# Kernel tuning notes

Hardware: AMD Instinct MI355X
Metric: run time of the kernel (lower is better)

Reference implementation:

```python
import jax, jax.numpy as jnp
import numpy as np

N_NODES = 100000
N_EDGES = 1600000
IN_FEATS = 64
H_FEATS = 64
NUM_CLASSES = 32


def _cgnn(h, e, src, dst, W, b, n_nodes):
    # message: m = h[src] * e  (e is [E,1], broadcasts over feature dim)
    m = h[src] * e  # [E, F]
    # segment mean over destination nodes (DGL fn.mean -> 0 for isolated nodes)
    s = jax.ops.segment_sum(m, dst, num_segments=n_nodes)  # [N, F]
    deg = jax.ops.segment_sum(jnp.ones((m.shape[0],), m.dtype), dst,
                              num_segments=n_nodes)  # [N]
    h_N = s / jnp.maximum(deg, 1.0)[:, None]
    h_total = jnp.concatenate([h, h_N], axis=1)  # [N, 2F]
    return h_total @ W + b


def setup_inputs() -> dict:
    key = jax.random.key(0)
    k = jax.random.split(key, 8)
    in_feat = jax.random.normal(k[0], (N_NODES, IN_FEATS), dtype=jnp.float32)
    edge_feat = jax.random.uniform(k[1], (N_EDGES, 1), dtype=jnp.float32)
    src = jax.random.randint(k[2], (N_EDGES,), 0, N_NODES)
    dst = jax.random.randint(k[3], (N_EDGES,), 0, N_NODES)
    # Linear(2*in_feats, h_feats) and Linear(2*h_feats, num_classes)
    s1 = 1.0 / np.sqrt(2 * IN_FEATS)
    s2 = 1.0 / np.sqrt(2 * H_FEATS)
    W1 = jax.random.uniform(k[4], (2 * IN_FEATS, H_FEATS), jnp.float32, -s1, s1)
    b1 = jax.random.uniform(k[5], (H_FEATS,), jnp.float32, -s1, s1)
    W2 = jax.random.uniform(k[6], (2 * H_FEATS, NUM_CLASSES), jnp.float32, -s2, s2)
    b2 = jax.random.uniform(k[7], (NUM_CLASSES,), jnp.float32, -s2, s2)
    return {"in_feat": in_feat, "edge_feat": edge_feat, "src": src,
            "dst": dst, "W1": W1, "b1": b1, "W2": W2, "b2": b2}


def reference(in_feat, edge_feat, src, dst, W1, b1, W2, b2):
    h = _cgnn(in_feat, edge_feat, src, dst, W1, b1, N_NODES)
    h = jax.nn.relu(h)
    h = _cgnn(h, edge_feat, src, dst, W2, b2, N_NODES)
    return h
```

## Files before the change

### kernel.cpp

```cpp
#include <hip/hip_runtime.h>
#include <hip/hip_bf16.h>


#define F 64
#define EPT 8
#define TPB 1024
#define EPB (EPT * TPB)
#define SBSHIFT 8
#define SBSZ 256
#define NSBMAX 512
#define PADSB 4864

__device__ __forceinline__ unsigned bf16_rne(float f)
{
    unsigned u = __float_as_uint(f);
    return (u + 0x7FFFu + ((u >> 16) & 1u)) >> 16;
}

__global__ __launch_bounds__(256) void cvt_init_kernel(
    const float* __restrict__ x, unsigned short* __restrict__ y, int n8,
    int* __restrict__ bcursor, int nsb)
{
    const int i = blockIdx.x * 256 + threadIdx.x;
    if (i < nsb) bcursor[i] = i * PADSB;
    if (i >= n8) return;
    const float4 a = ((const float4*)x)[2 * i];
    const float4 b = ((const float4*)x)[2 * i + 1];
    uint4 o;
    o.x = bf16_rne(a.x) | (bf16_rne(a.y) << 16);
    o.y = bf16_rne(a.z) | (bf16_rne(a.w) << 16);
    o.z = bf16_rne(b.x) | (bf16_rne(b.y) << 16);
    o.w = bf16_rne(b.z) | (bf16_rne(b.w) << 16);
    ((uint4*)y)[i] = o;
}

__global__ __launch_bounds__(TPB) void multisplit_kernel(
    const int* __restrict__ src, const int* __restrict__ dst,
    const float* __restrict__ ef, int* __restrict__ bcursor,
    int2* __restrict__ brec, int n_edges, int nsb)
{
    __shared__ int lcnt[NSBMAX];
    __shared__ int lbase[NSBMAX];
    const int tid = threadIdx.x;
    for (int i = tid; i < nsb; i += TPB) lcnt[i] = 0;
    __syncthreads();

    const int e0 = blockIdx.x * EPB + tid;
    int d[EPT], rk[EPT];
#pragma unroll
    for (int k = 0; k < EPT; ++k) {
        const int e = e0 + k * TPB;
        const int dd = (e < n_edges) ? dst[e] : -1;
        d[k]  = dd;
        rk[k] = (dd >= 0) ? atomicAdd(&lcnt[dd >> SBSHIFT], 1) : 0;
    }
    __syncthreads();
    for (int i = tid; i < nsb; i += TPB) {
        const int c = lcnt[i];
        lbase[i] = c ? atomicAdd(&bcursor[i], c) : 0;
    }
    __syncthreads();
#pragma unroll
    for (int k = 0; k < EPT; ++k) {
        const int e = e0 + k * TPB;
        if (e < n_edges) {
            const int dd  = d[k];
            const int bkt = dd >> SBSHIFT;
            const int pos = lbase[bkt] + rk[k];
            if (pos < (bkt + 1) * PADSB)
                brec[pos] = make_int2(((dd & (SBSZ - 1)) << 17) | src[e],
                                      __float_as_int(ef[e]));
        }
    }
}

__global__ __launch_bounds__(512) void bucket_sort_kernel(
    int2* __restrict__ brec, const int* __restrict__ bcursor,
    int* __restrict__ off2, int* __restrict__ end2,
    float* __restrict__ invdeg, int n_nodes)
{
    __shared__ int2 stage[PADSB];
    __shared__ int  lcnt[SBSZ];
    __shared__ int  lcur[SBSZ];
    __shared__ int  wsum[4];

    const int b   = blockIdx.x;
    const int tid = threadIdx.x;
    const int w0  = b * PADSB;
    int cnt = bcursor[b] - w0;
    if (cnt > PADSB) cnt = PADSB;

    if (tid < SBSZ) lcnt[tid] = 0;
    __syncthreads();

    for (int i = tid; i < cnt; i += 512) {
        const int2 r = brec[w0 + i];
        stage[i] = r;
        atomicAdd(&lcnt[r.x >> 17], 1);
    }
    __syncthreads();

    int v = 0, c = 0;
    if (tid < SBSZ) {
        c = lcnt[tid];
        v = c;
        for (int d = 1; d < 64; d <<= 1) {
            int t = __shfl_up(v, d, 64);
            if ((tid & 63) >= d) v += t;
        }
        if ((tid & 63) == 63) wsum[tid >> 6] = v;
    }
    __syncthreads();
    if (tid == 0) {
        int a = 0;
#pragma unroll
        for (int i = 0; i < 4; ++i) { int t = wsum[i]; wsum[i] = a; a += t; }
    }
    __syncthreads();
    if (tid < SBSZ) {
        const int excl = wsum[tid >> 6] + (v - c);
        lcur[tid] = excl;
        const int node = (b << SBSHIFT) + tid;
        if (node < n_nodes) {
            off2[node]   = w0 + excl;
            end2[node]   = w0 + excl + c;
            invdeg[node] = 1.0f / fmaxf((float)c, 1.0f);
        }
    }
    __syncthreads();

    for (int i = tid; i < cnt; i += 512) {
        const int2 r   = stage[i];
        const int  pos = atomicAdd(&lcur[r.x >> 17], 1);
        brec[w0 + pos] = make_int2((r.x & 0x1FFFF) << 6, r.y);
    }
}

__global__ __launch_bounds__(256) void agg_h_kernel(
    const unsigned short* __restrict__ hb, const int2* __restrict__ rec,
    const int* __restrict__ off, const int* __restrict__ end,
    const float* __restrict__ invdeg, unsigned short* __restrict__ sb,
    int n_nodes)
{
    const int wid  = (blockIdx.x * 256 + threadIdx.x) >> 6;
    const int lane = threadIdx.x & 63;
    const int n    = lane >> 5;
    const int r    = lane & 31;
    const int g    = r >> 3;
    const int q    = r & 7;

    const int  node   = wid * 2 + n;
    const bool active = node < n_nodes;
    const int  e0 = active ? off[node] : 0;
    const int  e1 = active ? end[node] : 0;

    const char* __restrict__ hq = (const char*)hb + q * 16;

    float4 aA0 = make_float4(0.f, 0.f, 0.f, 0.f);
    float4 aA1 = make_float4(0.f, 0.f, 0.f, 0.f);
    float4 aB0 = make_float4(0.f, 0.f, 0.f, 0.f);
    float4 aB1 = make_float4(0.f, 0.f, 0.f, 0.f);

    for (int base = e0; base < e1; base += 8) {
        const int  eA = base + g;
        const int  eB = base + 4 + g;
        const bool vA = eA < e1;
        const bool vB = eB < e1;
        const int2 rA = rec[vA ? eA : e0];
        const int2 rB = rec[vB ? eB : e0];
        const float evA = vA ? __int_as_float(rA.y) : 0.f;
        const float evB = vB ? __int_as_float(rB.y) : 0.f;
        const uint4 xA = *(const uint4*)(hq + ((size_t)(unsigned)rA.x << 1));
        const uint4 xB = *(const uint4*)(hq + ((size_t)(unsigned)rB.x << 1));

#define ACC8(xa, ev, lo, hi)                                         \
        lo.x = fmaf(__uint_as_float(xa.x << 16),         ev, lo.x);  \
        lo.y = fmaf(__uint_as_float(xa.x & 0xFFFF0000u), ev, lo.y);  \
        lo.z = fmaf(__uint_as_float(xa.y << 16),         ev, lo.z);  \
        lo.w = fmaf(__uint_as_float(xa.y & 0xFFFF0000u), ev, lo.w);  \
        hi.x = fmaf(__uint_as_float(xa.z << 16),         ev, hi.x);  \
        hi.y = fmaf(__uint_as_float(xa.z & 0xFFFF0000u), ev, hi.y);  \
        hi.z = fmaf(__uint_as_float(xa.w << 16),         ev, hi.z);  \
        hi.w = fmaf(__uint_as_float(xa.w & 0xFFFF0000u), ev, hi.w);

        ACC8(xA, evA, aA0, aA1)
        ACC8(xB, evB, aB0, aB1)
    }

    float4 a0 = make_float4(aA0.x + aB0.x, aA0.y + aB0.y,
                            aA0.z + aB0.z, aA0.w + aB0.w);
    float4 a1 = make_float4(aA1.x + aB1.x, aA1.y + aB1.y,
                            aA1.z + aB1.z, aA1.w + aB1.w);

#pragma unroll
    for (int m = 8; m <= 16; m <<= 1) {
        a0.x += __shfl_xor(a0.x, m); a0.y += __shfl_xor(a0.y, m);
        a0.z += __shfl_xor(a0.z, m); a0.w += __shfl_xor(a0.w, m);
        a1.x += __shfl_xor(a1.x, m); a1.y += __shfl_xor(a1.y, m);
        a1.z += __shfl_xor(a1.z, m); a1.w += __shfl_xor(a1.w, m);
    }

    if (g == 0 && active) {
        const float id = invdeg[node];
        uint4 o;
        o.x = bf16_rne(a0.x * id) | (bf16_rne(a0.y * id) << 16);
        o.y = bf16_rne(a0.z * id) | (bf16_rne(a0.w * id) << 16);
        o.z = bf16_rne(a1.x * id) | (bf16_rne(a1.y * id) << 16);
        o.w = bf16_rne(a1.z * id) | (bf16_rne(a1.w * id) << 16);
        *(uint4*)(sb + (size_t)node * F + q * 8) = o;
    }
}

__global__ __launch_bounds__(256) void agg_y_kernel(
    const unsigned short* __restrict__ yb, const int2* __restrict__ rec,
    const int* __restrict__ off, const int* __restrict__ end,
    const float* __restrict__ invdeg, unsigned short* __restrict__ s2b,
    int n_nodes)
{
    const int wid  = (blockIdx.x * 256 + threadIdx.x) >> 6;
    const int lane = threadIdx.x & 63;
    const int n    = lane >> 4;
    const int r    = lane & 15;
    const int g    = r >> 2;
    const int q    = r & 3;

    const int  node   = wid * 4 + n;
    const bool active = node < n_nodes;
    const int  e0 = active ? off[node] : 0;
    const int  e1 = active ? end[node] : 0;

    const char* __restrict__ hq = (const char*)yb + q * 16;

    float4 aA0 = make_float4(0.f, 0.f, 0.f, 0.f);
    float4 aA1 = make_float4(0.f, 0.f, 0.f, 0.f);
    float4 aB0 = make_float4(0.f, 0.f, 0.f, 0.f);
    float4 aB1 = make_float4(0.f, 0.f, 0.f, 0.f);

    for (int base = e0; base < e1; base += 8) {
        const int  eA = base + g;
        const int  eB = base + 4 + g;
        const bool vA = eA < e1;
        const bool vB = eB < e1;
        const int2 rA = rec[vA ? eA : e0];
        const int2 rB = rec[vB ? eB : e0];
        const float evA = vA ? __int_as_float(rA.y) : 0.f;
        const float evB = vB ? __int_as_float(rB.y) : 0.f;
        const uint4 xA = *(const uint4*)(hq + (size_t)(unsigned)rA.x);
        const uint4 xB = *(const uint4*)(hq + (size_t)(unsigned)rB.x);

        ACC8(xA, evA, aA0, aA1)
        ACC8(xB, evB, aB0, aB1)
    }

    float4 a0 = make_float4(aA0.x + aB0.x, aA0.y + aB0.y,
                            aA0.z + aB0.z, aA0.w + aB0.w);
    float4 a1 = make_float4(aA1.x + aB1.x, aA1.y + aB1.y,
                            aA1.z + aB1.z, aA1.w + aB1.w);

#pragma unroll
    for (int m = 4; m <= 8; m <<= 1) {
        a0.x += __shfl_xor(a0.x, m); a0.y += __shfl_xor(a0.y, m);
        a0.z += __shfl_xor(a0.z, m); a0.w += __shfl_xor(a0.w, m);
        a1.x += __shfl_xor(a1.x, m); a1.y += __shfl_xor(a1.y, m);
        a1.z += __shfl_xor(a1.z, m); a1.w += __shfl_xor(a1.w, m);
    }
#undef ACC8

    if (g == 0 && active) {
        const float id = invdeg[node];
        uint4 o;
        o.x = bf16_rne(a0.x * id) | (bf16_rne(a0.y * id) << 16);
        o.y = bf16_rne(a0.z * id) | (bf16_rne(a0.w * id) << 16);
        o.z = bf16_rne(a1.x * id) | (bf16_rne(a1.y * id) << 16);
        o.w = bf16_rne(a1.z * id) | (bf16_rne(a1.w * id) << 16);
        *(uint4*)(s2b + (size_t)node * 32 + q * 8) = o;
    }
}

template <int OUT, bool RELU, bool OUT_BF16>
__global__ __launch_bounds__(256) void linear_lds_kernel(
    const unsigned short* __restrict__ hin_b,
    const unsigned short* __restrict__ sb,
    const float* __restrict__ W, const float* __restrict__ b,
    float* __restrict__ out, unsigned short* __restrict__ hb_out, int n_nodes)
{
    constexpr int JT  = OUT / 4;
    constexpr int STR = 132;
    __shared__ float xin[64 * STR];

    const int tid   = threadIdx.x;
    const int node0 = blockIdx.x * 64;

#define STAGE_BF16(srcp, base_off, width)                                 \
    for (int i = tid; i < 64 * ((width) / 8); i += 256) {                 \
        const int ln = i / ((width) / 8), c8 = i % ((width) / 8);         \
        const int node = node0 + ln;                                      \
        uint4 v = make_uint4(0u, 0u, 0u, 0u);                             \
        if (node < n_nodes)                                               \
            v = *(const uint4*)&srcp[(size_t)node * (width) + c8 * 8];    \
        float4 lo = make_float4(__uint_as_float(v.x << 16),               \
                                __uint_as_float(v.x & 0xFFFF0000u),       \
                                __uint_as_float(v.y << 16),               \
                                __uint_as_float(v.y & 0xFFFF0000u));      \
        float4 hi = make_float4(__uint_as_float(v.z << 16),               \
                                __uint_as_float(v.z & 0xFFFF0000u),       \
                                __uint_as_float(v.w << 16),               \
                                __uint_as_float(v.w & 0xFFFF0000u));      \
        *(float4*)&xin[ln * STR + (base_off) + c8 * 8]     = lo;          \
        *(float4*)&xin[ln * STR + (base_off) + c8 * 8 + 4] = hi;          \
    }

    STAGE_BF16(hin_b, 0, 64)
    STAGE_BF16(sb,    F, 64)
    __syncthreads();

    const int lane = tid & 63;
    const int j0   = __builtin_amdgcn_readfirstlane((tid >> 6) * JT);

    float acc[JT];
#pragma unroll
    for (int j = 0; j < JT; ++j) acc[j] = b[j0 + j];

    const float* __restrict__ xrow = &xin[lane * STR];
#pragma unroll 2
    for (int k4 = 0; k4 < 32; ++k4) {
        const float4 xv = *(const float4*)&xrow[k4 * 4];
#pragma unroll
        for (int kk = 0; kk < 4; ++kk) {
            const int   k  = k4 * 4 + kk;
            const float xk = ((const float*)&xv)[kk];
#pragma unroll
            for (int j = 0; j < JT; ++j)
                acc[j] = fmaf(xk, W[k * OUT + j0 + j], acc[j]);
        }
    }

    const int node = node0 + lane;
    if (node < n_nodes) {
#pragma unroll
        for (int j = 0; j < JT; ++j) {
            float v = acc[j];
            if (RELU) v = fmaxf(v, 0.f);
            acc[j] = v;
        }
        if constexpr (OUT_BF16) {
            unsigned* __restrict__ hw =
                (unsigned*)(hb_out + (size_t)node * OUT + j0);
#pragma unroll
            for (int j = 0; j < JT; j += 2)
                hw[j >> 1] = bf16_rne(acc[j]) | (bf16_rne(acc[j + 1]) << 16);
        } else {
#pragma unroll
            for (int j = 0; j < JT; ++j)
                out[(size_t)node * OUT + j0 + j] = acc[j];
        }
    }
}

__global__ __launch_bounds__(256) void y2gemm_kernel(
    const unsigned short* __restrict__ hin_b, const float* __restrict__ Wb,
    unsigned short* __restrict__ yb2, int n_nodes)
{
    constexpr int STR = 68;
    __shared__ float xin[64 * STR];
    const int tid   = threadIdx.x;
    const int node0 = blockIdx.x * 64;

    STAGE_BF16(hin_b, 0, 64)
    __syncthreads();

    const int lane = tid & 63;
    const int j0   = __builtin_amdgcn_readfirstlane((tid >> 6) * 8);

    float acc[8];
#pragma unroll
    for (int j = 0; j < 8; ++j) acc[j] = 0.f;

    const float* __restrict__ xrow = &xin[lane * STR];
#pragma unroll 2
    for (int k4 = 0; k4 < 16; ++k4) {
        const float4 xv = *(const float4*)&xrow[k4 * 4];
#pragma unroll
        for (int kk = 0; kk < 4; ++kk) {
            const int   k  = k4 * 4 + kk;
            const float xk = ((const float*)&xv)[kk];
#pragma unroll
            for (int j = 0; j < 8; ++j)
                acc[j] = fmaf(xk, Wb[k * 32 + j0 + j], acc[j]);
        }
    }

    const int node = node0 + lane;
    if (node < n_nodes) {
        unsigned* __restrict__ hw = (unsigned*)(yb2 + (size_t)node * 32 + j0);
#pragma unroll
        for (int j = 0; j < 8; j += 2)
            hw[j >> 1] = bf16_rne(acc[j]) | (bf16_rne(acc[j + 1]) << 16);
    }
}

__global__ __launch_bounds__(256) void lin2h_kernel(
    const unsigned short* __restrict__ hin_b,
    const unsigned short* __restrict__ s2b,
    const float* __restrict__ Wt, const float* __restrict__ b,
    float* __restrict__ out, int n_nodes)
{
    constexpr int STR = 100;
    __shared__ float xin[64 * STR];
    const int tid   = threadIdx.x;
    const int node0 = blockIdx.x * 64;

    STAGE_BF16(hin_b, 0,  64)
    STAGE_BF16(s2b,   64, 32)
#undef STAGE_BF16
    __syncthreads();

    const int lane = tid & 63;
    const int j0   = __builtin_amdgcn_readfirstlane((tid >> 6) * 8);

    float acc[8];
#pragma unroll
    for (int j = 0; j < 8; ++j) acc[j] = b[j0 + j];

    const float* __restrict__ xrow = &xin[lane * STR];
#pragma unroll 2
    for (int k4 = 0; k4 < 16; ++k4) {
        const float4 xv = *(const float4*)&xrow[k4 * 4];
#pragma unroll
        for (int kk = 0; kk < 4; ++kk) {
            const int   k  = k4 * 4 + kk;
            const float xk = ((const float*)&xv)[kk];
#pragma unroll
            for (int j = 0; j < 8; ++j)
                acc[j] = fmaf(xk, Wt[k * 32 + j0 + j], acc[j]);
        }
    }

    const int node = node0 + lane;
    if (node < n_nodes) {
#pragma unroll
        for (int j = 0; j < 8; ++j)
            out[(size_t)node * 32 + j0 + j] = acc[j] + xrow[64 + j0 + j];
    }
}

extern "C" void kernel_launch(void* const* d_in, const int* in_sizes, int n_in,
                              void* d_out, int out_size, void* d_ws, size_t ws_size,
                              hipStream_t stream)
{
    const float* in_feat   = (const float*)d_in[0];
    const float* edge_feat = (const float*)d_in[1];
    const int*   src       = (const int*)d_in[2];
    const int*   dst       = (const int*)d_in[3];
    const float* W1        = (const float*)d_in[4];
    const float* b1        = (const float*)d_in[5];
    const float* W2        = (const float*)d_in[6];
    const float* b2        = (const float*)d_in[7];
    float*       out       = (float*)d_out;

    const int n_nodes = in_sizes[0] / F;
    const int n_edges = in_sizes[2];
    const int nsb     = (n_nodes + SBSZ - 1) >> SBSHIFT;

    const int S = 100352;
    int*   wsi     = (int*)d_ws;
    int*   bcursor = wsi;
    int*   off2    = wsi + 1024;
    int*   end2    = wsi + 1024 + S;
    float* invdeg  = (float*)(wsi + 1024 + 2 * S);
    int2*  brec    = (int2*)(wsi + 1024 + 3 * S);
    unsigned short* sb  = (unsigned short*)(brec + (size_t)nsb * PADSB);
    unsigned short* hb0 = sb  + (size_t)n_nodes * F;
    unsigned short* hb1 = hb0 + (size_t)n_nodes * F;
    unsigned short* yb2 = hb1 + (size_t)n_nodes * F;
    unsigned short* s2b = yb2 + (size_t)n_nodes * 32;

    const int n8     = (n_nodes * F) >> 3;
    const int cgrid  = (n8 + 255) / 256;
    const int egrid  = (n_edges + EPB - 1) / EPB;
    const int agrid1 = (n_nodes + 7) / 8;
    const int agrid2 = (n_nodes + 15) / 16;
    const int lgrid  = (n_nodes + 63) / 64;

    cvt_init_kernel<<<cgrid, 256, 0, stream>>>(in_feat, hb0, n8, bcursor, nsb);
    multisplit_kernel<<<egrid, TPB, 0, stream>>>(src, dst, edge_feat,
                                                 bcursor, brec, n_edges, nsb);
    bucket_sort_kernel<<<nsb, 512, 0, stream>>>(brec, bcursor, off2, end2,
                                                invdeg, n_nodes);

    agg_h_kernel<<<agrid1, 256, 0, stream>>>(hb0, brec, off2, end2, invdeg,
                                             sb, n_nodes);
    linear_lds_kernel<64, true, true><<<lgrid, 256, 0, stream>>>(
        hb0, sb, W1, b1, nullptr, hb1, n_nodes);

    y2gemm_kernel<<<lgrid, 256, 0, stream>>>(hb1, W2 + 64 * 32, yb2, n_nodes);
    agg_y_kernel<<<agrid2, 256, 0, stream>>>(yb2, brec, off2, end2, invdeg,
                                             s2b, n_nodes);
    lin2h_kernel<<<lgrid, 256, 0, stream>>>(hb1, s2b, W2, b2, out, n_nodes);
}
```

Measured before the change: 153.1 us.

## Pack edge records into 32-bit words and fuse layer-1 linear with y2 GEMM

Edge records are compressed from int2 (8 bytes) to a single 32-bit word holding a 17-bit source index and a 15-bit bf16 edge weight with the sign bit dropped. This halves record traffic in both aggregation passes. The layer-1 linear+ReLU kernel now also computes the h1·W2b projection from LDS, which removes a separate kernel launch and a re-read of hb1. The cost is extra rounding of edge weights to bf16 and a reliance on edge weights being non-negative and node indices fitting in 17 bits.

```diff
diff --git a/kernel.cpp b/kernel.cpp
--- a/kernel.cpp
+++ b/kernel.cpp
@@ -15,6 +15,11 @@
 {
     unsigned u = __float_as_uint(f);
     return (u + 0x7FFFu + ((u >> 16) & 1u)) >> 16;
+}
+
+__device__ __forceinline__ float rec_ef(unsigned rec)
+{
+    return __uint_as_float((rec & 0xFFFE0000u) >> 1);
 }
 
 __global__ __launch_bounds__(256) void cvt_init_kernel(
@@ -75,9 +80,9 @@
 }
 
 __global__ __launch_bounds__(512) void bucket_sort_kernel(
-    int2* __restrict__ brec, const int* __restrict__ bcursor,
-    int* __restrict__ off2, int* __restrict__ end2,
-    float* __restrict__ invdeg, int n_nodes)
+    const int2* __restrict__ brec, const int* __restrict__ bcursor,
+    unsigned* __restrict__ rec2, int* __restrict__ off2,
+    int* __restrict__ end2, float* __restrict__ invdeg, int n_nodes)
 {
     __shared__ int2 stage[PADSB];
     __shared__ int  lcnt[SBSZ];
@@ -132,12 +137,13 @@
     for (int i = tid; i < cnt; i += 512) {
         const int2 r   = stage[i];
         const int  pos = atomicAdd(&lcur[r.x >> 17], 1);
-        brec[w0 + pos] = make_int2((r.x & 0x1FFFF) << 6, r.y);
+        const unsigned ef15 = bf16_rne(__int_as_float(r.y)) & 0x7FFFu;
+        rec2[w0 + pos] = (ef15 << 17) | (unsigned)(r.x & 0x1FFFF);
     }
 }
 
 __global__ __launch_bounds__(256) void agg_h_kernel(
-    const unsigned short* __restrict__ hb, const int2* __restrict__ rec,
+    const unsigned short* __restrict__ hb, const unsigned* __restrict__ rec,
     const int* __restrict__ off, const int* __restrict__ end,
     const float* __restrict__ invdeg, unsigned short* __restrict__ sb,
     int n_nodes)
@@ -166,12 +172,12 @@
         const int  eB = base + 4 + g;
         const bool vA = eA < e1;
         const bool vB = eB < e1;
-        const int2 rA = rec[vA ? eA : e0];
-        const int2 rB = rec[vB ? eB : e0];
-        const float evA = vA ? __int_as_float(rA.y) : 0.f;
-        const float evB = vB ? __int_as_float(rB.y) : 0.f;
-        const uint4 xA = *(const uint4*)(hq + ((size_t)(unsigned)rA.x << 1));
-        const uint4 xB = *(const uint4*)(hq + ((size_t)(unsigned)rB.x << 1));
+        const unsigned rA = rec[vA ? eA : e0];
+        const unsigned rB = rec[vB ? eB : e0];
+        const float evA = vA ? rec_ef(rA) : 0.f;
+        const float evB = vB ? rec_ef(rB) : 0.f;
+        const uint4 xA = *(const uint4*)(hq + ((size_t)(rA & 0x1FFFFu) << 7));
+        const uint4 xB = *(const uint4*)(hq + ((size_t)(rB & 0x1FFFFu) << 7));
 
 #define ACC8(xa, ev, lo, hi)                                         \
         lo.x = fmaf(__uint_as_float(xa.x << 16),         ev, lo.x);  \
@@ -212,7 +218,7 @@
 }
 
 __global__ __launch_bounds__(256) void agg_y_kernel(
-    const unsigned short* __restrict__ yb, const int2* __restrict__ rec,
+    const unsigned short* __restrict__ yb, const unsigned* __restrict__ rec,
     const int* __restrict__ off, const int* __restrict__ end,
     const float* __restrict__ invdeg, unsigned short* __restrict__ s2b,
     int n_nodes)
@@ -241,16 +247,17 @@
         const int  eB = base + 4 + g;
         const bool vA = eA < e1;
         const bool vB = eB < e1;
-        const int2 rA = rec[vA ? eA : e0];
-        const int2 rB = rec[vB ? eB : e0];
-        const float evA = vA ? __int_as_float(rA.y) : 0.f;
-        const float evB = vB ? __int_as_float(rB.y) : 0.f;
-        const uint4 xA = *(const uint4*)(hq + (size_t)(unsigned)rA.x);
-        const uint4 xB = *(const uint4*)(hq + (size_t)(unsigned)rB.x);
+        const unsigned rA = rec[vA ? eA : e0];
+        const unsigned rB = rec[vB ? eB : e0];
+        const float evA = vA ? rec_ef(rA) : 0.f;
+        const float evB = vB ? rec_ef(rB) : 0.f;
+        const uint4 xA = *(const uint4*)(hq + ((size_t)(rA & 0x1FFFFu) << 6));
+        const uint4 xB = *(const uint4*)(hq + ((size_t)(rB & 0x1FFFFu) << 6));
 
         ACC8(xA, evA, aA0, aA1)
         ACC8(xB, evB, aB0, aB1)
     }
+#undef ACC8
 
     float4 a0 = make_float4(aA0.x + aB0.x, aA0.y + aB0.y,
                             aA0.z + aB0.z, aA0.w + aB0.w);
@@ -264,7 +271,6 @@
         a1.x += __shfl_xor(a1.x, m); a1.y += __shfl_xor(a1.y, m);
         a1.z += __shfl_xor(a1.z, m); a1.w += __shfl_xor(a1.w, m);
     }
-#undef ACC8
 
     if (g == 0 && active) {
         const float id = invdeg[node];
@@ -277,49 +283,56 @@
     }
 }
 
-template <int OUT, bool RELU, bool OUT_BF16>
-__global__ __launch_bounds__(256) void linear_lds_kernel(
-    const unsigned short* __restrict__ hin_b,
+template <int WIDTH>
+__device__ __forceinline__ void stage_rows_bf16(
+    const unsigned short* __restrict__ srcp, float* __restrict__ xin,
+    int node0, int n_nodes, int tid, int stride, int base_off)
+{
+    constexpr int C8 = WIDTH / 8;
+    for (int i = tid; i < 64 * C8; i += 256) {
+        const int ln = i / C8, c8 = i % C8;
+        const int node = node0 + ln;
+        uint4 v = make_uint4(0u, 0u, 0u, 0u);
+        if (node < n_nodes)
+            v = *(const uint4*)&srcp[(size_t)node * WIDTH + c8 * 8];
+        float4 lo = make_float4(__uint_as_float(v.x << 16),
+                                __uint_as_float(v.x & 0xFFFF0000u),
+                                __uint_as_float(v.y << 16),
+                                __uint_as_float(v.y & 0xFFFF0000u));
+        float4 hi = make_float4(__uint_as_float(v.z << 16),
+                                __uint_as_float(v.z & 0xFFFF0000u),
+                                __uint_as_float(v.w << 16),
+                                __uint_as_float(v.w & 0xFFFF0000u));
+        *(float4*)&xin[ln * stride + base_off + c8 * 8]     = lo;
+        *(float4*)&xin[ln * stride + base_off + c8 * 8 + 4] = hi;
+    }
+}
+
+__global__ __launch_bounds__(256) void lin1_fused_kernel(
+    const unsigned short* __restrict__ hb0,
     const unsigned short* __restrict__ sb,
-    const float* __restrict__ W, const float* __restrict__ b,
-    float* __restrict__ out, unsigned short* __restrict__ hb_out, int n_nodes)
-{
-    constexpr int JT  = OUT / 4;
+    const float* __restrict__ W1, const float* __restrict__ b1,
+    const float* __restrict__ Wb,
+    unsigned short* __restrict__ hb1, unsigned short* __restrict__ yb2,
+    int n_nodes)
+{
     constexpr int STR = 132;
     __shared__ float xin[64 * STR];
 
     const int tid   = threadIdx.x;
     const int node0 = blockIdx.x * 64;
 
-#define STAGE_BF16(srcp, base_off, width)                                 \
-    for (int i = tid; i < 64 * ((width) / 8); i += 256) {                 \
-        const int ln = i / ((width) / 8), c8 = i % ((width) / 8);         \
-        const int node = node0 + ln;                                      \
-        uint4 v = make_uint4(0u, 0u, 0u, 0u);                             \
-        if (node < n_nodes)                                               \
-            v = *(const uint4*)&srcp[(size_t)node * (width) + c8 * 8];    \
-        float4 lo = make_float4(__uint_as_float(v.x << 16),               \
-                                __uint_as_float(v.x & 0xFFFF0000u),       \
-                                __uint_as_float(v.y << 16),               \
-                                __uint_as_float(v.y & 0xFFFF0000u));      \
-        float4 hi = make_float4(__uint_as_float(v.z << 16),               \
-                                __uint_as_float(v.z & 0xFFFF0000u),       \
-                                __uint_as_float(v.w << 16),               \
-                                __uint_as_float(v.w & 0xFFFF0000u));      \
-        *(float4*)&xin[ln * STR + (base_off) + c8 * 8]     = lo;          \
-        *(float4*)&xin[ln * STR + (base_off) + c8 * 8 + 4] = hi;          \
-    }
-
-    STAGE_BF16(hin_b, 0, 64)
-    STAGE_BF16(sb,    F, 64)
+    stage_rows_bf16<64>(hb0, xin, node0, n_nodes, tid, STR, 0);
+    stage_rows_bf16<64>(sb,  xin, node0, n_nodes, tid, STR, F);
     __syncthreads();
 
     const int lane = tid & 63;
-    const int j0   = __builtin_amdgcn_readfirstlane((tid >> 6) * JT);
-
-    float acc[JT];
-#pragma unroll
-    for (int j = 0; j < JT; ++j) acc[j] = b[j0 + j];
+    const int wv   = tid >> 6;
+    const int j0   = __builtin_amdgcn_readfirstlane(wv * 16);
+
+    float acc[16];
+#pragma unroll
+    for (int j = 0; j < 16; ++j) acc[j] = b1[j0 + j];
 
     const float* __restrict__ xrow = &xin[lane * STR];
 #pragma unroll 2
@@ -330,53 +343,34 @@
             const int   k  = k4 * 4 + kk;
             const float xk = ((const float*)&xv)[kk];
 #pragma unroll
-            for (int j = 0; j < JT; ++j)
-                acc[j] = fmaf(xk, W[k * OUT + j0 + j], acc[j]);
-        }
-    }
+            for (int j = 0; j < 16; ++j)
+                acc[j] = fmaf(xk, W1[k * 64 + j0 + j], acc[j]);
+        }
+    }
+
+#pragma unroll
+    for (int j = 0; j < 16; ++j) acc[j] = fmaxf(acc[j], 0.f);
 
     const int node = node0 + lane;
     if (node < n_nodes) {
-#pragma unroll
-        for (int j = 0; j < JT; ++j) {
-            float v = acc[j];
-            if (RELU) v = fmaxf(v, 0.f);
-            acc[j] = v;
-        }
-        if constexpr (OUT_BF16) {
-            unsigned* __restrict__ hw =
-                (unsigned*)(hb_out + (size_t)node * OUT + j0);
-#pragma unroll
-            for (int j = 0; j < JT; j += 2)
-                hw[j >> 1] = bf16_rne(acc[j]) | (bf16_rne(acc[j + 1]) << 16);
-        } else {
-#pragma unroll
-            for (int j = 0; j < JT; ++j)
-                out[(size_t)node * OUT + j0 + j] = acc[j];
-        }
-    }
-}
-
-__global__ __launch_bounds__(256) void y2gemm_kernel(
-    const unsigned short* __restrict__ hin_b, const float* __restrict__ Wb,
-    unsigned short* __restrict__ yb2, int n_nodes)
-{
-    constexpr int STR = 68;
-    __shared__ float xin[64 * STR];
-    const int tid   = threadIdx.x;
-    const int node0 = blockIdx.x * 64;
-
-    STAGE_BF16(hin_b, 0, 64)
-    __syncthreads();
-
-    const int lane = tid & 63;
-    const int j0   = __builtin_amdgcn_readfirstlane((tid >> 6) * 8);
-
-    float acc[8];
-#pragma unroll
-    for (int j = 0; j < 8; ++j) acc[j] = 0.f;
-
-    const float* __restrict__ xrow = &xin[lane * STR];
+        unsigned* __restrict__ hw = (unsigned*)(hb1 + (size_t)node * F + j0);
+#pragma unroll
+        for (int j = 0; j < 16; j += 2)
+            hw[j >> 1] = bf16_rne(acc[j]) | (bf16_rne(acc[j + 1]) << 16);
+    }
+
+    __syncthreads();
+    float* __restrict__ hrow_w = &xin[lane * STR + j0];
+#pragma unroll
+    for (int j = 0; j < 16; j += 4)
+        *(float4*)&hrow_w[j] = make_float4(acc[j], acc[j+1], acc[j+2], acc[j+3]);
+    __syncthreads();
+
+    const int j0y = __builtin_amdgcn_readfirstlane(wv * 8);
+    float acy[8];
+#pragma unroll
+    for (int j = 0; j < 8; ++j) acy[j] = 0.f;
+
 #pragma unroll 2
     for (int k4 = 0; k4 < 16; ++k4) {
         const float4 xv = *(const float4*)&xrow[k4 * 4];
@@ -386,16 +380,15 @@
             const float xk = ((const float*)&xv)[kk];
 #pragma unroll
             for (int j = 0; j < 8; ++j)
-                acc[j] = fmaf(xk, Wb[k * 32 + j0 + j], acc[j]);
-        }
-    }
-
-    const int node = node0 + lane;
+                acy[j] = fmaf(xk, Wb[k * 32 + j0y + j], acy[j]);
+        }
+    }
+
     if (node < n_nodes) {
-        unsigned* __restrict__ hw = (unsigned*)(yb2 + (size_t)node * 32 + j0);
+        unsigned* __restrict__ yw = (unsigned*)(yb2 + (size_t)node * 32 + j0y);
 #pragma unroll
         for (int j = 0; j < 8; j += 2)
-            hw[j >> 1] = bf16_rne(acc[j]) | (bf16_rne(acc[j + 1]) << 16);
+            yw[j >> 1] = bf16_rne(acy[j]) | (bf16_rne(acy[j + 1]) << 16);
     }
 }
 
@@ -410,9 +403,8 @@
     const int tid   = threadIdx.x;
     const int node0 = blockIdx.x * 64;
 
-    STAGE_BF16(hin_b, 0,  64)
-    STAGE_BF16(s2b,   64, 32)
-#undef STAGE_BF16
+    stage_rows_bf16<64>(hin_b, xin, node0, n_nodes, tid, STR, 0);
+    stage_rows_bf16<32>(s2b,   xin, node0, n_nodes, tid, STR, 64);
     __syncthreads();
 
     const int lane = tid & 63;
@@ -463,13 +455,14 @@
     const int nsb     = (n_nodes + SBSZ - 1) >> SBSHIFT;
 
     const int S = 100352;
-    int*   wsi     = (int*)d_ws;
-    int*   bcursor = wsi;
-    int*   off2    = wsi + 1024;
-    int*   end2    = wsi + 1024 + S;
-    float* invdeg  = (float*)(wsi + 1024 + 2 * S);
-    int2*  brec    = (int2*)(wsi + 1024 + 3 * S);
-    unsigned short* sb  = (unsigned short*)(brec + (size_t)nsb * PADSB);
+    int*      wsi     = (int*)d_ws;
+    int*      bcursor = wsi;
+    int*      off2    = wsi + 1024;
+    int*      end2    = wsi + 1024 + S;
+    float*    invdeg  = (float*)(wsi + 1024 + 2 * S);
+    int2*     brec    = (int2*)(wsi + 1024 + 3 * S);
+    unsigned* rec2    = (unsigned*)(brec + (size_t)nsb * PADSB);
+    unsigned short* sb  = (unsigned short*)(rec2 + (size_t)nsb * PADSB);
     unsigned short* hb0 = sb  + (size_t)n_nodes * F;
     unsigned short* hb1 = hb0 + (size_t)n_nodes * F;
     unsigned short* yb2 = hb1 + (size_t)n_nodes * F;
@@ -485,16 +478,16 @@
     cvt_init_kernel<<<cgrid, 256, 0, stream>>>(in_feat, hb0, n8, bcursor, nsb);
     multisplit_kernel<<<egrid, TPB, 0, stream>>>(src, dst, edge_feat,
                                                  bcursor, brec, n_edges, nsb);
-    bucket_sort_kernel<<<nsb, 512, 0, stream>>>(brec, bcursor, off2, end2,
-                                                invdeg, n_nodes);
-
-    agg_h_kernel<<<agrid1, 256, 0, stream>>>(hb0, brec, off2, end2, invdeg,
+    bucket_sort_kernel<<<nsb, 512, 0, stream>>>(brec, bcursor, rec2, off2,
+                                                end2, invdeg, n_nodes);
+
+    agg_h_kernel<<<agrid1, 256, 0, stream>>>(hb0, rec2, off2, end2, invdeg,
                                              sb, n_nodes);
-    linear_lds_kernel<64, true, true><<<lgrid, 256, 0, stream>>>(
-        hb0, sb, W1, b1, nullptr, hb1, n_nodes);
-
-    y2gemm_kernel<<<lgrid, 256, 0, stream>>>(hb1, W2 + 64 * 32, yb2, n_nodes);
-    agg_y_kernel<<<agrid2, 256, 0, stream>>>(yb2, brec, off2, end2, invdeg,
+    lin1_fused_kernel<<<lgrid, 256, 0, stream>>>(hb0, sb, W1, b1,
+                                                 W2 + 64 * 32, hb1, yb2,
+                                                 n_nodes);
+
+    agg_y_kernel<<<agrid2, 256, 0, stream>>>(yb2, rec2, off2, end2, invdeg,
                                              s2b, n_nodes);
     lin2h_kernel<<<lgrid, 256, 0, stream>>>(hb1, s2b, W2, b2, out, n_nodes);
 }
```

Result: slower. 164.9 us (+7.7%).
